# Performance work log

Hardware: AMD Instinct MI355X
Metric: run time of the kernel (lower is better)

The kernel has to match this reference:

```python
import jax, jax.numpy as jnp
import numpy as np

K = 2          # neighbors per point (init default k=2)
ALPHA = 5e-4   # regularization weight (init default)
N_CLASSES = 1000


def setup_inputs() -> dict:
    key = jax.random.key(0)
    k1, k2, k3 = jax.random.split(key, 3)
    n, d_feat, n_cls = 4096, 1024, N_CLASSES
    x_batch = jax.random.normal(k1, (n, d_feat), dtype=jnp.float32)
    y_batch = jax.random.randint(k2, (n,), 0, n_cls, dtype=jnp.int32)
    y_output = jax.random.normal(k3, (n, n_cls), dtype=jnp.float32)
    return {"x_batch": x_batch, "y_batch": y_batch, "y_output": y_output}


def _pairwise_dist(a):
    # ||a_i - a_j|| via gram trick; clamp for numerical safety.
    sq = jnp.sum(a * a, axis=-1)                       # [n]
    d2 = sq[:, None] + sq[None, :] - 2.0 * (a @ a.T)   # [n, n]
    d2 = jnp.maximum(d2, 0.0)
    # sqrt with zero-safe gradient (diag / coincident points)
    safe = jnp.where(d2 > 0.0, d2, 1.0)
    return jnp.where(d2 > 0.0, jnp.sqrt(safe), 0.0)


def reference(x_batch, y_batch, y_output):
    n = x_batch.shape[0]
    d = _pairwise_dist(x_batch)                        # [n, n] input-space distances

    # K nearest neighbors, excluding self (i != j in the original loops)
    d_knn = d + jnp.where(jnp.eye(n, dtype=bool), jnp.inf, 0.0)
    _, nbr_idx = jax.lax.top_k(-d_knn, K)              # [n, K] smallest distances
    nbr_mask = jnp.zeros((n, n), dtype=d.dtype)
    nbr_mask = nbr_mask.at[jnp.arange(n)[:, None], nbr_idx].set(1.0)

    same_class = (y_batch[:, None] == y_batch[None, :])
    w = jnp.exp(-d) * nbr_mask                         # exp(-d) on KNN edges only
    # w_diff = w_int - w_pen: +exp(-d) for same-class neighbors, -exp(-d) otherwise
    w_diff = jnp.where(same_class, w, -w)

    y_norm = _pairwise_dist(y_output)                  # [n, n] ||y_out_i - y_out_j||
    reg_value = jnp.sum(w_diff * y_norm)
    return ALPHA * reg_value
```

## Files before the change

kernel.cpp:

```cpp
#include <hip/hip_runtime.h>
#include <math.h>

#define ALPHA 5e-4f
#define BIG 1e30f

typedef __attribute__((ext_vector_type(8))) short bf16x8;
typedef __attribute__((ext_vector_type(4))) float f32x4;

__device__ __forceinline__ unsigned short f2bf(float x) {
    unsigned u = __builtin_bit_cast(unsigned, x);
    unsigned r = (u + 0x7FFFu + ((u >> 16) & 1u)) >> 16;
    return (unsigned short)r;
}
__device__ __forceinline__ float bf2f(unsigned short b) {
    unsigned u = ((unsigned)b) << 16;
    return __builtin_bit_cast(float, u);
}

__device__ __forceinline__ void gload16(const short* g, short* l) {
    __builtin_amdgcn_global_load_lds(
        (const __attribute__((address_space(1))) void*)g,
        (__attribute__((address_space(3))) void*)l, 16, 0, 0);
}

__global__ __launch_bounds__(256)
void conv_rownorm_kernel(const float* __restrict__ X, short* __restrict__ Xb,
                         float* __restrict__ sqn, int d) {
    const int w = threadIdx.x >> 6, lane = threadIdx.x & 63;
    const int row = blockIdx.x * 4 + w;
    const float4* src = reinterpret_cast<const float4*>(X + (size_t)row * d);
    short4* dst = reinterpret_cast<short4*>(Xb + (size_t)row * d);
    float s = 0.f;
    const int nv = d >> 2;
    for (int c = lane; c < nv; c += 64) {
        float4 v = src[c];
        unsigned short b0 = f2bf(v.x), b1 = f2bf(v.y), b2 = f2bf(v.z), b3 = f2bf(v.w);
        float x0 = bf2f(b0), x1 = bf2f(b1), x2 = bf2f(b2), x3 = bf2f(b3);
        s += x0 * x0 + x1 * x1 + x2 * x2 + x3 * x3;
        dst[c] = make_short4((short)b0, (short)b1, (short)b2, (short)b3);
    }
    for (int off = 1; off < 64; off <<= 1) s += __shfl_xor(s, off, 64);
    if (lane == 0) sqn[row] = s;
}

#define BM 128
#define BN 128
#define BK 32

__global__ __launch_bounds__(256)
void gram_top2_mfma(const short* __restrict__ Xb, const float* __restrict__ sqn,
                    float* __restrict__ cand_s, int* __restrict__ cand_i,
                    int n, int d, int nb, int cpx) {
    __shared__ short As[3][BM * BK];
    __shared__ short Bs[3][BN * BK];

    const int nwg = nb * (nb + 1) / 2;
    int bid = blockIdx.x;
    int swz = (bid & 7) * cpx + (bid >> 3);
    (void)nwg;
    int rb = 0, rem = swz;
    while (rem >= nb - rb) { rem -= nb - rb; ++rb; }
    const int cb = rb + rem;

    const int row0 = rb * BM, col0 = cb * BN;
    const int t = threadIdx.x;
    const int w = t >> 6, l = t & 63;
    const int wr = w >> 1, wc = w & 1;
    const int lc = l & 15, lg = l >> 4;

    f32x4 acc[4][4];
#pragma unroll
    for (int i = 0; i < 4; ++i)
#pragma unroll
        for (int j = 0; j < 4; ++j) acc[i][j] = (f32x4){0.f, 0.f, 0.f, 0.f};

    const int gchunk = (t & 3) ^ ((t >> 3) & 3);
    const size_t gA0 = (size_t)(row0 + (t >> 2)) * d + gchunk * 8;
    const size_t gB0 = (size_t)(col0 + (t >> 2)) * d + gchunk * 8;
    const size_t rstep = (size_t)64 * d;
    const int kswz = (lg ^ ((lc >> 1) & 3)) * 8;
    const int wbase = w * 512;

    const int nsteps = d / BK;

    {
        short* la = As[0] + wbase;  short* lb = Bs[0] + wbase;
        gload16(Xb + gA0, la);          gload16(Xb + gA0 + rstep, la + 2048);
        gload16(Xb + gB0, lb);          gload16(Xb + gB0 + rstep, lb + 2048);
        la = As[1] + wbase;  lb = Bs[1] + wbase;
        gload16(Xb + gA0 + BK, la);     gload16(Xb + gA0 + BK + rstep, la + 2048);
        gload16(Xb + gB0 + BK, lb);     gload16(Xb + gB0 + BK + rstep, lb + 2048);
    }

    int s0 = 0, s1 = 1, s2 = 2;
    for (int ks = 0; ks < nsteps; ++ks) {
        if (ks + 2 < nsteps) {
            short* la = As[s2] + wbase;  short* lb = Bs[s2] + wbase;
            const size_t ko = (size_t)(ks + 2) * BK;
            gload16(Xb + gA0 + ko, la);      gload16(Xb + gA0 + ko + rstep, la + 2048);
            gload16(Xb + gB0 + ko, lb);      gload16(Xb + gB0 + ko + rstep, lb + 2048);
            asm volatile("s_waitcnt vmcnt(8)" ::: "memory");
        } else if (ks + 1 < nsteps) {
            asm volatile("s_waitcnt vmcnt(4)" ::: "memory");
        } else {
            asm volatile("s_waitcnt vmcnt(0)" ::: "memory");
        }
        __builtin_amdgcn_s_barrier();

        bf16x8 a[4], b[4];
#pragma unroll
        for (int mi = 0; mi < 4; ++mi)
            a[mi] = *reinterpret_cast<const bf16x8*>(&As[s0][(wr * 64 + mi * 16 + lc) * BK + kswz]);
#pragma unroll
        for (int ni = 0; ni < 4; ++ni)
            b[ni] = *reinterpret_cast<const bf16x8*>(&Bs[s0][(wc * 64 + ni * 16 + lc) * BK + kswz]);
#pragma unroll
        for (int mi = 0; mi < 4; ++mi)
#pragma unroll
            for (int ni = 0; ni < 4; ++ni)
                acc[mi][ni] = __builtin_amdgcn_mfma_f32_16x16x32_bf16(
                    a[mi], b[ni], acc[mi][ni], 0, 0, 0);

        asm volatile("s_waitcnt lgkmcnt(0)" ::: "memory");
        __builtin_amdgcn_s_barrier();
        int tmp = s0; s0 = s1; s1 = s2; s2 = tmp;
    }

    float sq_c[4];
#pragma unroll
    for (int ni = 0; ni < 4; ++ni) sq_c[ni] = sqn[col0 + wc * 64 + ni * 16 + lc];
    const int strip_r = cb * 2 + wc;

#pragma unroll
    for (int mi = 0; mi < 4; ++mi) {
#pragma unroll
        for (int j = 0; j < 4; ++j) {
            const int grow = row0 + wr * 64 + mi * 16 + lg * 4 + j;
            float s1v = BIG, s2v = BIG;
            int i1 = -1, i2 = -1;
#pragma unroll
            for (int ni = 0; ni < 4; ++ni) {
                const int gcol = col0 + wc * 64 + ni * 16 + lc;
                float s = sq_c[ni] - 2.f * acc[mi][ni][j];
                if (gcol == grow) s = BIG;
                if (s < s1v) { s2v = s1v; i2 = i1; s1v = s; i1 = gcol; }
                else if (s < s2v) { s2v = s; i2 = gcol; }
            }
            for (int off = 1; off < 16; off <<= 1) {
                float b1 = __shfl_xor(s1v, off, 16);
                int  bi1 = __shfl_xor(i1, off, 16);
                float b2 = __shfl_xor(s2v, off, 16);
                int  bi2 = __shfl_xor(i2, off, 16);
                if (b1 < s1v) { s2v = s1v; i2 = i1; s1v = b1; i1 = bi1; }
                else if (b1 < s2v) { s2v = b1; i2 = bi1; }
                if (b2 < s2v) { s2v = b2; i2 = bi2; }
            }
            if (lc == 0) {
                size_t base = ((size_t)grow * 64 + strip_r) * 2;
                cand_s[base] = s1v; cand_s[base + 1] = s2v;
                cand_i[base] = i1; cand_i[base + 1] = i2;
            }
        }
    }

    if (rb != cb) {
        float sq_r[4][4];
#pragma unroll
        for (int mi = 0; mi < 4; ++mi)
#pragma unroll
            for (int j = 0; j < 4; ++j)
                sq_r[mi][j] = sqn[row0 + wr * 64 + mi * 16 + lg * 4 + j];
        const int strip_c = rb * 2 + wr;

#pragma unroll
        for (int ni = 0; ni < 4; ++ni) {
            const int gcol = col0 + wc * 64 + ni * 16 + lc;
            float s1v = BIG, s2v = BIG;
            int i1 = -1, i2 = -1;
#pragma unroll
            for (int mi = 0; mi < 4; ++mi)
#pragma unroll
                for (int j = 0; j < 4; ++j) {
                    const int grow = row0 + wr * 64 + mi * 16 + lg * 4 + j;
                    float s = sq_r[mi][j] - 2.f * acc[mi][ni][j];
                    if (s < s1v) { s2v = s1v; i2 = i1; s1v = s; i1 = grow; }
                    else if (s < s2v) { s2v = s; i2 = grow; }
                }
#pragma unroll
            for (int off = 16; off < 64; off <<= 1) {
                float b1 = __shfl_xor(s1v, off, 64);
                int  bi1 = __shfl_xor(i1, off, 64);
                float b2 = __shfl_xor(s2v, off, 64);
                int  bi2 = __shfl_xor(i2, off, 64);
                if (b1 < s1v) { s2v = s1v; i2 = i1; s1v = b1; i1 = bi1; }
                else if (b1 < s2v) { s2v = b1; i2 = bi1; }
                if (b2 < s2v) { s2v = b2; i2 = bi2; }
            }
            if (lg == 0) {
                size_t base = ((size_t)gcol * 64 + strip_c) * 2;
                cand_s[base] = s1v; cand_s[base + 1] = s2v;
                cand_i[base] = i1; cand_i[base + 1] = i2;
            }
        }
    }
}

__global__ __launch_bounds__(256)
void merge_edges_kernel(const float* __restrict__ sqn,
                        const float* __restrict__ cand_s, const int* __restrict__ cand_i,
                        const int* __restrict__ yb, const float* __restrict__ yo,
                        float* __restrict__ partial, int ncls) {
    const int w = threadIdx.x >> 6, lane = threadIdx.x & 63;
    const int row = blockIdx.x * 4 + w;

    float2 cs = reinterpret_cast<const float2*>(cand_s + (size_t)row * 128)[lane];
    int2   ci = reinterpret_cast<const int2*>(cand_i + (size_t)row * 128)[lane];
    float s1 = cs.x, s2 = cs.y;
    int i1 = ci.x, i2 = ci.y;
    if (s2 < s1) { float ts = s1; s1 = s2; s2 = ts; int ti = i1; i1 = i2; i2 = ti; }

    for (int off = 1; off < 64; off <<= 1) {
        float b1 = __shfl_xor(s1, off, 64);
        int  bi1 = __shfl_xor(i1, off, 64);
        float b2 = __shfl_xor(s2, off, 64);
        int  bi2 = __shfl_xor(i2, off, 64);
        if (b1 < s1) { s2 = s1; i2 = i1; s1 = b1; i1 = bi1; }
        else if (b1 < s2) { s2 = b1; i2 = bi1; }
        if (b2 < s2) { s2 = b2; i2 = bi2; }
    }
    const int yr = yb[row];
    const float sr = sqn[row];
    float w1 = ((yr == yb[i1]) ? 1.f : -1.f) * expf(-sqrtf(fmaxf(sr + s1, 0.f)));
    float w2 = ((yr == yb[i2]) ? 1.f : -1.f) * expf(-sqrtf(fmaxf(sr + s2, 0.f)));

    const float4* yr4 = reinterpret_cast<const float4*>(yo + (size_t)row * ncls);
    const float4* y14 = reinterpret_cast<const float4*>(yo + (size_t)i1 * ncls);
    const float4* y24 = reinterpret_cast<const float4*>(yo + (size_t)i2 * ncls);
    const int nv4 = ncls >> 2;
    float a1 = 0.f, a2 = 0.f;
    for (int c = lane; c < nv4; c += 64) {
        float4 v = yr4[c];
        float4 u1 = y14[c];
        float4 u2 = y24[c];
        float tx = v.x - u1.x, ty = v.y - u1.y, tz = v.z - u1.z, tw = v.w - u1.w;
        a1 = fmaf(tx, tx, fmaf(ty, ty, fmaf(tz, tz, fmaf(tw, tw, a1))));
        tx = v.x - u2.x; ty = v.y - u2.y; tz = v.z - u2.z; tw = v.w - u2.w;
        a2 = fmaf(tx, tx, fmaf(ty, ty, fmaf(tz, tz, fmaf(tw, tw, a2))));
    }
    for (int c = (nv4 << 2) + lane; c < ncls; c += 64) {
        float v = yo[(size_t)row * ncls + c];
        float t1 = v - yo[(size_t)i1 * ncls + c];
        float t2 = v - yo[(size_t)i2 * ncls + c];
        a1 = fmaf(t1, t1, a1);
        a2 = fmaf(t2, t2, a2);
    }
    for (int off = 1; off < 64; off <<= 1) {
        a1 += __shfl_xor(a1, off, 64);
        a2 += __shfl_xor(a2, off, 64);
    }
    if (lane == 0)
        partial[row] = w1 * sqrtf(a1) + w2 * sqrtf(a2);
}

__global__ __launch_bounds__(256)
void final_reduce_kernel(const float* __restrict__ partial, float* __restrict__ out, int n) {
    const int t = threadIdx.x;
    __shared__ float red[4];
    float s = 0.f;
    const int nv4 = n >> 2;
    const float4* p4 = reinterpret_cast<const float4*>(partial);
    for (int c = t; c < nv4; c += 256) {
        float4 v = p4[c];
        s += v.x + v.y + v.z + v.w;
    }
    for (int off = 1; off < 64; off <<= 1) s += __shfl_xor(s, off, 64);
    if ((t & 63) == 0) red[t >> 6] = s;
    __syncthreads();
    if (t == 0) out[0] = ALPHA * (red[0] + red[1] + red[2] + red[3]);
}

extern "C" void kernel_launch(void* const* d_in, const int* in_sizes, int n_in,
                              void* d_out, int out_size, void* d_ws, size_t ws_size,
                              hipStream_t stream) {
    const float* X  = (const float*)d_in[0];
    const int*   yb = (const int*)d_in[1];
    const float* yo = (const float*)d_in[2];
    float* out = (float*)d_out;

    const int n    = in_sizes[1];
    const int d    = in_sizes[0] / n;
    const int ncls = in_sizes[2] / n;
    const int nb   = n / BM;

    char* wsb = (char*)d_ws;
    size_t off = 0;
    float* sqn = (float*)(wsb + off);    off += ((size_t)n * 4 + 255) & ~(size_t)255;
    short* Xb  = (short*)(wsb + off);    off += ((size_t)n * d * 2 + 255) & ~(size_t)255;
    float* cand_s = (float*)(wsb + off); off += ((size_t)n * 64 * 2 * 4 + 255) & ~(size_t)255;
    int*   cand_i = (int*)(wsb + off);   off += ((size_t)n * 64 * 2 * 4 + 255) & ~(size_t)255;
    float* partial = (float*)(wsb + off);

    conv_rownorm_kernel<<<n / 4, 256, 0, stream>>>(X, Xb, sqn, d);

    const int ntri = nb * (nb + 1) / 2;
    const int cpx  = ntri / 8;
    gram_top2_mfma<<<ntri, 256, 0, stream>>>(Xb, sqn, cand_s, cand_i, n, d, nb, cpx);

    merge_edges_kernel<<<n / 4, 256, 0, stream>>>(sqn, cand_s, cand_i, yb, yo, partial, ncls);

    final_reduce_kernel<<<1, 256, 0, stream>>>(partial, out, n);
}
```

Measured before the change: 60.67 us.

## Enlarge gram tile to 256x256 with 512-thread blocks and 8 waves

Doubles the gram/top-2 tile from 128x128 to 256x256, using 8 waves in a 2x4 layout where each wave accumulates a 128x64 sub-tile. Each loaded element is reused across more output, so global and LDS traffic per FLOP drops. Only 136 workgroups are launched for n=4096, so the launch no longer fills all CUs of the MI355X. Register pressure also rises with 128 accumulator floats per thread, and row norms are now read from global memory inside the column-candidate loop.

New measurement: 82.63 us. 1.36x slower.

```diff
diff --git a/kernel.cpp b/kernel.cpp
--- a/kernel.cpp
+++ b/kernel.cpp
@@ -43,53 +43,50 @@
     if (lane == 0) sqn[row] = s;
 }
 
-#define BM 128
-#define BN 128
+#define BM 256
+#define BN 256
 #define BK 32
 
-__global__ __launch_bounds__(256)
+__global__ __launch_bounds__(512, 2)
 void gram_top2_mfma(const short* __restrict__ Xb, const float* __restrict__ sqn,
                     float* __restrict__ cand_s, int* __restrict__ cand_i,
                     int n, int d, int nb, int cpx) {
     __shared__ short As[3][BM * BK];
     __shared__ short Bs[3][BN * BK];
 
-    const int nwg = nb * (nb + 1) / 2;
-    int bid = blockIdx.x;
-    int swz = (bid & 7) * cpx + (bid >> 3);
-    (void)nwg;
-    int rb = 0, rem = swz;
+    const int bid = blockIdx.x;
+    int rem = (bid & 7) * cpx + (bid >> 3);
+    int rb = 0;
     while (rem >= nb - rb) { rem -= nb - rb; ++rb; }
     const int cb = rb + rem;
 
     const int row0 = rb * BM, col0 = cb * BN;
     const int t = threadIdx.x;
     const int w = t >> 6, l = t & 63;
-    const int wr = w >> 1, wc = w & 1;
+    const int wr = w >> 2, wcn = w & 3;
     const int lc = l & 15, lg = l >> 4;
 
-    f32x4 acc[4][4];
-#pragma unroll
-    for (int i = 0; i < 4; ++i)
+    f32x4 acc[8][4];
+#pragma unroll
+    for (int i = 0; i < 8; ++i)
 #pragma unroll
         for (int j = 0; j < 4; ++j) acc[i][j] = (f32x4){0.f, 0.f, 0.f, 0.f};
 
     const int gchunk = (t & 3) ^ ((t >> 3) & 3);
     const size_t gA0 = (size_t)(row0 + (t >> 2)) * d + gchunk * 8;
     const size_t gB0 = (size_t)(col0 + (t >> 2)) * d + gchunk * 8;
-    const size_t rstep = (size_t)64 * d;
+    const size_t rstep = (size_t)128 * d;
     const int kswz = (lg ^ ((lc >> 1) & 3)) * 8;
     const int wbase = w * 512;
 
     const int nsteps = d / BK;
 
-    {
-        short* la = As[0] + wbase;  short* lb = Bs[0] + wbase;
-        gload16(Xb + gA0, la);          gload16(Xb + gA0 + rstep, la + 2048);
-        gload16(Xb + gB0, lb);          gload16(Xb + gB0 + rstep, lb + 2048);
-        la = As[1] + wbase;  lb = Bs[1] + wbase;
-        gload16(Xb + gA0 + BK, la);     gload16(Xb + gA0 + BK + rstep, la + 2048);
-        gload16(Xb + gB0 + BK, lb);     gload16(Xb + gB0 + BK + rstep, lb + 2048);
+#pragma unroll
+    for (int s = 0; s < 2; ++s) {
+        short* la = As[s] + wbase;  short* lb = Bs[s] + wbase;
+        const size_t ko = (size_t)s * BK;
+        gload16(Xb + gA0 + ko, la);        gload16(Xb + gA0 + ko + rstep, la + 4096);
+        gload16(Xb + gB0 + ko, lb);        gload16(Xb + gB0 + ko + rstep, lb + 4096);
     }
 
     int s0 = 0, s1 = 1, s2 = 2;
@@ -97,8 +94,8 @@
         if (ks + 2 < nsteps) {
             short* la = As[s2] + wbase;  short* lb = Bs[s2] + wbase;
             const size_t ko = (size_t)(ks + 2) * BK;
-            gload16(Xb + gA0 + ko, la);      gload16(Xb + gA0 + ko + rstep, la + 2048);
-            gload16(Xb + gB0 + ko, lb);      gload16(Xb + gB0 + ko + rstep, lb + 2048);
+            gload16(Xb + gA0 + ko, la);    gload16(Xb + gA0 + ko + rstep, la + 4096);
+            gload16(Xb + gB0 + ko, lb);    gload16(Xb + gB0 + ko + rstep, lb + 4096);
             asm volatile("s_waitcnt vmcnt(8)" ::: "memory");
         } else if (ks + 1 < nsteps) {
             asm volatile("s_waitcnt vmcnt(4)" ::: "memory");
@@ -107,15 +104,15 @@
         }
         __builtin_amdgcn_s_barrier();
 
-        bf16x8 a[4], b[4];
-#pragma unroll
-        for (int mi = 0; mi < 4; ++mi)
-            a[mi] = *reinterpret_cast<const bf16x8*>(&As[s0][(wr * 64 + mi * 16 + lc) * BK + kswz]);
+        bf16x8 a[8], b[4];
+#pragma unroll
+        for (int mi = 0; mi < 8; ++mi)
+            a[mi] = *reinterpret_cast<const bf16x8*>(&As[s0][(wr * 128 + mi * 16 + lc) * BK + kswz]);
 #pragma unroll
         for (int ni = 0; ni < 4; ++ni)
-            b[ni] = *reinterpret_cast<const bf16x8*>(&Bs[s0][(wc * 64 + ni * 16 + lc) * BK + kswz]);
-#pragma unroll
-        for (int mi = 0; mi < 4; ++mi)
+            b[ni] = *reinterpret_cast<const bf16x8*>(&Bs[s0][(wcn * 64 + ni * 16 + lc) * BK + kswz]);
+#pragma unroll
+        for (int mi = 0; mi < 8; ++mi)
 #pragma unroll
             for (int ni = 0; ni < 4; ++ni)
                 acc[mi][ni] = __builtin_amdgcn_mfma_f32_16x16x32_bf16(
@@ -128,19 +125,19 @@
 
     float sq_c[4];
 #pragma unroll
-    for (int ni = 0; ni < 4; ++ni) sq_c[ni] = sqn[col0 + wc * 64 + ni * 16 + lc];
-    const int strip_r = cb * 2 + wc;
-
-#pragma unroll
-    for (int mi = 0; mi < 4; ++mi) {
+    for (int ni = 0; ni < 4; ++ni) sq_c[ni] = sqn[col0 + wcn * 64 + ni * 16 + lc];
+    const int strip_r = cb * 4 + wcn;
+
+#pragma unroll
+    for (int mi = 0; mi < 8; ++mi) {
 #pragma unroll
         for (int j = 0; j < 4; ++j) {
-            const int grow = row0 + wr * 64 + mi * 16 + lg * 4 + j;
+            const int grow = row0 + wr * 128 + mi * 16 + lg * 4 + j;
             float s1v = BIG, s2v = BIG;
             int i1 = -1, i2 = -1;
 #pragma unroll
             for (int ni = 0; ni < 4; ++ni) {
-                const int gcol = col0 + wc * 64 + ni * 16 + lc;
+                const int gcol = col0 + wcn * 64 + ni * 16 + lc;
                 float s = sq_c[ni] - 2.f * acc[mi][ni][j];
                 if (gcol == grow) s = BIG;
                 if (s < s1v) { s2v = s1v; i2 = i1; s1v = s; i1 = gcol; }
@@ -164,42 +161,40 @@
     }
 
     if (rb != cb) {
-        float sq_r[4][4];
-#pragma unroll
-        for (int mi = 0; mi < 4; ++mi)
-#pragma unroll
-            for (int j = 0; j < 4; ++j)
-                sq_r[mi][j] = sqn[row0 + wr * 64 + mi * 16 + lg * 4 + j];
-        const int strip_c = rb * 2 + wr;
-
-#pragma unroll
-        for (int ni = 0; ni < 4; ++ni) {
-            const int gcol = col0 + wc * 64 + ni * 16 + lc;
-            float s1v = BIG, s2v = BIG;
-            int i1 = -1, i2 = -1;
-#pragma unroll
-            for (int mi = 0; mi < 4; ++mi)
-#pragma unroll
-                for (int j = 0; j < 4; ++j) {
-                    const int grow = row0 + wr * 64 + mi * 16 + lg * 4 + j;
-                    float s = sq_r[mi][j] - 2.f * acc[mi][ni][j];
-                    if (s < s1v) { s2v = s1v; i2 = i1; s1v = s; i1 = grow; }
-                    else if (s < s2v) { s2v = s; i2 = grow; }
+#pragma unroll
+        for (int half = 0; half < 2; ++half) {
+            const int strip_c = rb * 4 + wr * 2 + half;
+#pragma unroll
+            for (int ni = 0; ni < 4; ++ni) {
+                const int gcol = col0 + wcn * 64 + ni * 16 + lc;
+                float s1v = BIG, s2v = BIG;
+                int i1 = -1, i2 = -1;
+#pragma unroll
+                for (int mq = 0; mq < 4; ++mq) {
+                    const int mi = half * 4 + mq;
+#pragma unroll
+                    for (int j = 0; j < 4; ++j) {
+                        const int grow = row0 + wr * 128 + mi * 16 + lg * 4 + j;
+                        float s = sqn[grow] - 2.f * acc[mi][ni][j];
+                        if (s < s1v) { s2v = s1v; i2 = i1; s1v = s; i1 = grow; }
+                        else if (s < s2v) { s2v = s; i2 = grow; }
+                    }
                 }
 #pragma unroll
-            for (int off = 16; off < 64; off <<= 1) {
-                float b1 = __shfl_xor(s1v, off, 64);
-                int  bi1 = __shfl_xor(i1, off, 64);
-                float b2 = __shfl_xor(s2v, off, 64);
-                int  bi2 = __shfl_xor(i2, off, 64);
-                if (b1 < s1v) { s2v = s1v; i2 = i1; s1v = b1; i1 = bi1; }
-                else if (b1 < s2v) { s2v = b1; i2 = bi1; }
-                if (b2 < s2v) { s2v = b2; i2 = bi2; }
-            }
-            if (lg == 0) {
-                size_t base = ((size_t)gcol * 64 + strip_c) * 2;
-                cand_s[base] = s1v; cand_s[base + 1] = s2v;
-                cand_i[base] = i1; cand_i[base + 1] = i2;
+                for (int off = 16; off < 64; off <<= 1) {
+                    float b1 = __shfl_xor(s1v, off, 64);
+                    int  bi1 = __shfl_xor(i1, off, 64);
+                    float b2 = __shfl_xor(s2v, off, 64);
+                    int  bi2 = __shfl_xor(i2, off, 64);
+                    if (b1 < s1v) { s2v = s1v; i2 = i1; s1v = b1; i1 = bi1; }
+                    else if (b1 < s2v) { s2v = b1; i2 = bi1; }
+                    if (b2 < s2v) { s2v = b2; i2 = bi2; }
+                }
+                if (lg == 0) {
+                    size_t base = ((size_t)gcol * 64 + strip_c) * 2;
+                    cand_s[base] = s1v; cand_s[base + 1] = s2v;
+                    cand_i[base] = i1; cand_i[base + 1] = i2;
+                }
             }
         }
     }
@@ -304,7 +299,7 @@
 
     const int ntri = nb * (nb + 1) / 2;
     const int cpx  = ntri / 8;
-    gram_top2_mfma<<<ntri, 256, 0, stream>>>(Xb, sqn, cand_s, cand_i, n, d, nb, cpx);
+    gram_top2_mfma<<<ntri, 512, 0, stream>>>(Xb, sqn, cand_s, cand_i, n, d, nb, cpx);
 
     merge_edges_kernel<<<n / 4, 256, 0, stream>>>(sqn, cand_s, cand_i, yb, yo, partial, ncls);
 
```

## Use 512-thread gram tiles with 2x4 wave layout and wider candidate slots

Applied to the files above, without the earlier changes.

Doubles the gram kernel's workgroup to 8 waves, each computing a 64x32 sub-tile instead of 64x64. Each thread now issues one global-to-LDS load per matrix per K step, and the vmcnt waits are adjusted to match. MFMA sections are wrapped in s_setprio, and the candidate layout grows to 128 slots per row, with the merge kernel masking unused slots. The aim is more waves for latency hiding and less register pressure, at the cost of more LDS reads per MFMA, more candidate traffic and a larger merge input.

Result: slower. 64.85 us (+6.9%).

```diff
diff --git a/kernel.cpp b/kernel.cpp
--- a/kernel.cpp
+++ b/kernel.cpp
@@ -47,89 +47,85 @@
 #define BN 128
 #define BK 32
 
-__global__ __launch_bounds__(256)
+__global__ __launch_bounds__(512, 4)
 void gram_top2_mfma(const short* __restrict__ Xb, const float* __restrict__ sqn,
                     float* __restrict__ cand_s, int* __restrict__ cand_i,
                     int n, int d, int nb, int cpx) {
     __shared__ short As[3][BM * BK];
     __shared__ short Bs[3][BN * BK];
 
-    const int nwg = nb * (nb + 1) / 2;
-    int bid = blockIdx.x;
-    int swz = (bid & 7) * cpx + (bid >> 3);
-    (void)nwg;
-    int rb = 0, rem = swz;
+    const int bid = blockIdx.x;
+    int rem = (bid & 7) * cpx + (bid >> 3);
+    int rb = 0;
     while (rem >= nb - rb) { rem -= nb - rb; ++rb; }
     const int cb = rb + rem;
 
     const int row0 = rb * BM, col0 = cb * BN;
     const int t = threadIdx.x;
     const int w = t >> 6, l = t & 63;
-    const int wr = w >> 1, wc = w & 1;
+    const int wr = w >> 2, wcn = w & 3;
     const int lc = l & 15, lg = l >> 4;
 
-    f32x4 acc[4][4];
+    f32x4 acc[4][2];
 #pragma unroll
     for (int i = 0; i < 4; ++i)
 #pragma unroll
-        for (int j = 0; j < 4; ++j) acc[i][j] = (f32x4){0.f, 0.f, 0.f, 0.f};
+        for (int j = 0; j < 2; ++j) acc[i][j] = (f32x4){0.f, 0.f, 0.f, 0.f};
 
     const int gchunk = (t & 3) ^ ((t >> 3) & 3);
     const size_t gA0 = (size_t)(row0 + (t >> 2)) * d + gchunk * 8;
     const size_t gB0 = (size_t)(col0 + (t >> 2)) * d + gchunk * 8;
-    const size_t rstep = (size_t)64 * d;
     const int kswz = (lg ^ ((lc >> 1) & 3)) * 8;
     const int wbase = w * 512;
 
     const int nsteps = d / BK;
 
-    {
-        short* la = As[0] + wbase;  short* lb = Bs[0] + wbase;
-        gload16(Xb + gA0, la);          gload16(Xb + gA0 + rstep, la + 2048);
-        gload16(Xb + gB0, lb);          gload16(Xb + gB0 + rstep, lb + 2048);
-        la = As[1] + wbase;  lb = Bs[1] + wbase;
-        gload16(Xb + gA0 + BK, la);     gload16(Xb + gA0 + BK + rstep, la + 2048);
-        gload16(Xb + gB0 + BK, lb);     gload16(Xb + gB0 + BK + rstep, lb + 2048);
+#pragma unroll
+    for (int s = 0; s < 2; ++s) {
+        gload16(Xb + gA0 + s * BK, As[s] + wbase);
+        gload16(Xb + gB0 + s * BK, Bs[s] + wbase);
     }
 
     int s0 = 0, s1 = 1, s2 = 2;
     for (int ks = 0; ks < nsteps; ++ks) {
         if (ks + 2 < nsteps) {
-            short* la = As[s2] + wbase;  short* lb = Bs[s2] + wbase;
             const size_t ko = (size_t)(ks + 2) * BK;
-            gload16(Xb + gA0 + ko, la);      gload16(Xb + gA0 + ko + rstep, la + 2048);
-            gload16(Xb + gB0 + ko, lb);      gload16(Xb + gB0 + ko + rstep, lb + 2048);
-            asm volatile("s_waitcnt vmcnt(8)" ::: "memory");
+            gload16(Xb + gA0 + ko, As[s2] + wbase);
+            gload16(Xb + gB0 + ko, Bs[s2] + wbase);
+            asm volatile("s_waitcnt vmcnt(4)" ::: "memory");
         } else if (ks + 1 < nsteps) {
-            asm volatile("s_waitcnt vmcnt(4)" ::: "memory");
+            asm volatile("s_waitcnt vmcnt(2)" ::: "memory");
         } else {
             asm volatile("s_waitcnt vmcnt(0)" ::: "memory");
         }
         __builtin_amdgcn_s_barrier();
 
-        bf16x8 a[4], b[4];
+        bf16x8 a[4], b[2];
 #pragma unroll
         for (int mi = 0; mi < 4; ++mi)
             a[mi] = *reinterpret_cast<const bf16x8*>(&As[s0][(wr * 64 + mi * 16 + lc) * BK + kswz]);
 #pragma unroll
-        for (int ni = 0; ni < 4; ++ni)
-            b[ni] = *reinterpret_cast<const bf16x8*>(&Bs[s0][(wc * 64 + ni * 16 + lc) * BK + kswz]);
+        for (int ni = 0; ni < 2; ++ni)
+            b[ni] = *reinterpret_cast<const bf16x8*>(&Bs[s0][(wcn * 32 + ni * 16 + lc) * BK + kswz]);
+
+        __builtin_amdgcn_s_setprio(1);
 #pragma unroll
         for (int mi = 0; mi < 4; ++mi)
 #pragma unroll
-            for (int ni = 0; ni < 4; ++ni)
+            for (int ni = 0; ni < 2; ++ni)
                 acc[mi][ni] = __builtin_amdgcn_mfma_f32_16x16x32_bf16(
                     a[mi], b[ni], acc[mi][ni], 0, 0, 0);
+        __builtin_amdgcn_s_setprio(0);
 
         asm volatile("s_waitcnt lgkmcnt(0)" ::: "memory");
         __builtin_amdgcn_s_barrier();
         int tmp = s0; s0 = s1; s1 = s2; s2 = tmp;
     }
 
-    float sq_c[4];
-#pragma unroll
-    for (int ni = 0; ni < 4; ++ni) sq_c[ni] = sqn[col0 + wc * 64 + ni * 16 + lc];
-    const int strip_r = cb * 2 + wc;
+    float sq_c[2];
+#pragma unroll
+    for (int ni = 0; ni < 2; ++ni) sq_c[ni] = sqn[col0 + wcn * 32 + ni * 16 + lc];
+    const int slot_r = 2 * rb + (cb - rb) * 4 + wcn;
 
 #pragma unroll
     for (int mi = 0; mi < 4; ++mi) {
@@ -139,8 +135,8 @@
             float s1v = BIG, s2v = BIG;
             int i1 = -1, i2 = -1;
 #pragma unroll
-            for (int ni = 0; ni < 4; ++ni) {
-                const int gcol = col0 + wc * 64 + ni * 16 + lc;
+            for (int ni = 0; ni < 2; ++ni) {
+                const int gcol = col0 + wcn * 32 + ni * 16 + lc;
                 float s = sq_c[ni] - 2.f * acc[mi][ni][j];
                 if (gcol == grow) s = BIG;
                 if (s < s1v) { s2v = s1v; i2 = i1; s1v = s; i1 = gcol; }
@@ -156,7 +152,7 @@
                 if (b2 < s2v) { s2v = b2; i2 = bi2; }
             }
             if (lc == 0) {
-                size_t base = ((size_t)grow * 64 + strip_r) * 2;
+                size_t base = ((size_t)grow * 128 + slot_r) * 2;
                 cand_s[base] = s1v; cand_s[base + 1] = s2v;
                 cand_i[base] = i1; cand_i[base + 1] = i2;
             }
@@ -170,11 +166,11 @@
 #pragma unroll
             for (int j = 0; j < 4; ++j)
                 sq_r[mi][j] = sqn[row0 + wr * 64 + mi * 16 + lg * 4 + j];
-        const int strip_c = rb * 2 + wr;
-
-#pragma unroll
-        for (int ni = 0; ni < 4; ++ni) {
-            const int gcol = col0 + wc * 64 + ni * 16 + lc;
+        const int slot_c = rb * 2 + wr;
+
+#pragma unroll
+        for (int ni = 0; ni < 2; ++ni) {
+            const int gcol = col0 + wcn * 32 + ni * 16 + lc;
             float s1v = BIG, s2v = BIG;
             int i1 = -1, i2 = -1;
 #pragma unroll
@@ -197,7 +193,7 @@
                 if (b2 < s2v) { s2v = b2; i2 = bi2; }
             }
             if (lg == 0) {
-                size_t base = ((size_t)gcol * 64 + strip_c) * 2;
+                size_t base = ((size_t)gcol * 128 + slot_c) * 2;
                 cand_s[base] = s1v; cand_s[base + 1] = s2v;
                 cand_i[base] = i1; cand_i[base + 1] = i2;
             }
@@ -212,12 +208,23 @@
                         float* __restrict__ partial, int ncls) {
     const int w = threadIdx.x >> 6, lane = threadIdx.x & 63;
     const int row = blockIdx.x * 4 + w;
-
-    float2 cs = reinterpret_cast<const float2*>(cand_s + (size_t)row * 128)[lane];
-    int2   ci = reinterpret_cast<const int2*>(cand_i + (size_t)row * 128)[lane];
-    float s1 = cs.x, s2 = cs.y;
-    int i1 = ci.x, i2 = ci.y;
-    if (s2 < s1) { float ts = s1; s1 = s2; s2 = ts; int ti = i1; i1 = i2; i2 = ti; }
+    const int valid = 128 - 2 * (row >> 7);
+
+    float4 cs = reinterpret_cast<const float4*>(cand_s + (size_t)row * 256)[lane];
+    int4   ci = reinterpret_cast<const int4*>(cand_i + (size_t)row * 256)[lane];
+    float s1a = cs.x, s2a = cs.y, s1b = cs.z, s2b = cs.w;
+    int   i1a = ci.x, i2a = ci.y, i1b = ci.z, i2b = ci.w;
+    if (2 * lane     >= valid) { s1a = BIG; s2a = BIG; i1a = -1; i2a = -1; }
+    if (2 * lane + 1 >= valid) { s1b = BIG; s2b = BIG; i1b = -1; i2b = -1; }
+
+    float s1, s2; int i1, i2;
+    if (s1b < s1a) {
+        s1 = s1b; i1 = i1b;
+        if (s1a < s2b) { s2 = s1a; i2 = i1a; } else { s2 = s2b; i2 = i2b; }
+    } else {
+        s1 = s1a; i1 = i1a;
+        if (s1b < s2a) { s2 = s1b; i2 = i1b; } else { s2 = s2a; i2 = i2a; }
+    }
 
     for (int off = 1; off < 64; off <<= 1) {
         float b1 = __shfl_xor(s1, off, 64);
@@ -296,15 +303,15 @@
     size_t off = 0;
     float* sqn = (float*)(wsb + off);    off += ((size_t)n * 4 + 255) & ~(size_t)255;
     short* Xb  = (short*)(wsb + off);    off += ((size_t)n * d * 2 + 255) & ~(size_t)255;
-    float* cand_s = (float*)(wsb + off); off += ((size_t)n * 64 * 2 * 4 + 255) & ~(size_t)255;
-    int*   cand_i = (int*)(wsb + off);   off += ((size_t)n * 64 * 2 * 4 + 255) & ~(size_t)255;
+    float* cand_s = (float*)(wsb + off); off += ((size_t)n * 128 * 2 * 4 + 255) & ~(size_t)255;
+    int*   cand_i = (int*)(wsb + off);   off += ((size_t)n * 128 * 2 * 4 + 255) & ~(size_t)255;
     float* partial = (float*)(wsb + off);
 
     conv_rownorm_kernel<<<n / 4, 256, 0, stream>>>(X, Xb, sqn, d);
 
     const int ntri = nb * (nb + 1) / 2;
     const int cpx  = ntri / 8;
-    gram_top2_mfma<<<ntri, 256, 0, stream>>>(Xb, sqn, cand_s, cand_i, n, d, nb, cpx);
+    gram_top2_mfma<<<ntri, 512, 0, stream>>>(Xb, sqn, cand_s, cand_i, n, d, nb, cpx);
 
     merge_edges_kernel<<<n / 4, 256, 0, stream>>>(sqn, cand_s, cand_i, yb, yo, partial, ncls);
 
```
